# Performance work log

Measured on AMD Instinct MI355X. Metric: run time of the kernel, lower is better.

Reference implementation:

```python
import jax, jax.numpy as jnp
import numpy as np

NUM_HEADS = 16

def setup_inputs() -> dict:
    key = jax.random.key(0)
    kq, kk, kv = jax.random.split(key, 3)
    B, S, D = 4, 2048, 1024
    return {
        "queries": jax.random.normal(kq, (B, S, D), dtype=jnp.float32),
        "keys": jax.random.normal(kk, (B, S, D), dtype=jnp.float32),
        "values": jax.random.normal(kv, (B, S, D), dtype=jnp.float32),
    }

def _split_heads(x):
    # [B, S, D] -> [B, H, S, Dh]
    B, S, D = x.shape
    return x.reshape(B, S, NUM_HEADS, D // NUM_HEADS).transpose(0, 2, 1, 3)

def reference(queries, keys, values):
    q = _split_heads(queries)   # [B, H, S, Dh]
    k = _split_heads(keys)
    v = _split_heads(values)
    d_k = k.shape[-1]
    scale = 1.0 / jnp.sqrt(jnp.asarray(d_k, dtype=q.dtype))
    # [B, H, S, S] score matrix (materialized, as in the original bmm path)
    scores = jnp.einsum('bhqd,bhkd->bhqk', q, k) * scale
    weights = jax.nn.softmax(scores, axis=-1)
    out = jnp.einsum('bhqk,bhkd->bhqd', weights, v)  # [B, H, S, Dh]
    B, H, S, Dh = out.shape
    return out.transpose(0, 2, 1, 3).reshape(B, S, H * Dh)
```

## Files before the change

kernel.cpp:

```cpp
#include <hip/hip_runtime.h>
#include <hip/hip_bf16.h>
#include <math.h>

#define SEQ    2048
#define NH     16
#define DH     64
#define DMODEL 1024
#define KT     64
#define NT     (SEQ/KT)
#define KH_BYTES (4 * NH * SEQ * DH * 2)

typedef __bf16 bf16x8 __attribute__((ext_vector_type(8)));
typedef float  f32x4  __attribute__((ext_vector_type(4)));
typedef float  f32x16 __attribute__((ext_vector_type(16)));
typedef unsigned u32x2 __attribute__((ext_vector_type(2)));
typedef unsigned short u16x8 __attribute__((ext_vector_type(8)));
typedef __attribute__((address_space(3))) unsigned int        lds_u32_t;
typedef __attribute__((address_space(1))) const unsigned int  g_u32_t;

__device__ __forceinline__ ushort f2bf(float f) {
    union { __hip_bfloat16 h; ushort u; } z;
    z.h = __float2bfloat16(f);
    return z.u;
}

__device__ __forceinline__ unsigned pk2(float lo, float hi) {
    unsigned r;
    asm("v_cvt_pk_bf16_f32 %0, %1, %2" : "=v"(r) : "v"(lo), "v"(hi));
    return r;
}

__device__ __forceinline__ float fexp2(float x) {
#if __has_builtin(__builtin_amdgcn_exp2f)
    return __builtin_amdgcn_exp2f(x);
#else
    float r; asm("v_exp_f32 %0, %1\n\ts_nop 0" : "=v"(r) : "v"(x)); return r;
#endif
}

__device__ __forceinline__ void load16(const char* g, char* l) {
    __builtin_amdgcn_global_load_lds((g_u32_t*)g, (lds_u32_t*)l, 16, 0, 0);
}

__global__ __launch_bounds__(256)
void prep_kv(const float* __restrict__ K, const float* __restrict__ V,
             ushort* __restrict__ Kh, ushort* __restrict__ Vt) {
    __shared__ __attribute__((aligned(16))) ushort T[64 * 64];
    int blk = blockIdx.x;
    int tid = threadIdx.x;
    if (blk < 2048) {
        int i = tid >> 6;
        int c = tid & 63;
        int g = blk * 4 + i;
        int b = g >> 11, s = g & 2047;
        int h = c >> 2, d0 = (c & 3) * 16;
        const float* kp = K + (size_t)g * DMODEL + c * 16;
        float4 f0 = ((const float4*)kp)[0];
        float4 f1 = ((const float4*)kp)[1];
        float4 f2 = ((const float4*)kp)[2];
        float4 f3 = ((const float4*)kp)[3];
        u16x8 a, bq;
        a[0]=f2bf(f0.x); a[1]=f2bf(f0.y); a[2]=f2bf(f0.z); a[3]=f2bf(f0.w);
        a[4]=f2bf(f1.x); a[5]=f2bf(f1.y); a[6]=f2bf(f1.z); a[7]=f2bf(f1.w);
        bq[0]=f2bf(f2.x); bq[1]=f2bf(f2.y); bq[2]=f2bf(f2.z); bq[3]=f2bf(f2.w);
        bq[4]=f2bf(f3.x); bq[5]=f2bf(f3.y); bq[6]=f2bf(f3.z); bq[7]=f2bf(f3.w);
        ushort* op = Kh + ((size_t)(b * NH + h) * SEQ + s) * DH + d0;
        *(u16x8*)op = a;
        *(u16x8*)(op + 8) = bq;
    } else {
        int vb = blk - 2048;
        int st = vb & 31, bh = vb >> 5;
        int b = bh >> 4, h = bh & 15;
        int s0 = st * 64;
        char* TB = (char*)T;
        {
            int sr = tid >> 2, seg = tid & 3;
            const float* vp = V + ((size_t)(b * SEQ + s0 + sr)) * DMODEL + h * DH + seg * 16;
            float4 f0 = ((const float4*)vp)[0];
            float4 f1 = ((const float4*)vp)[1];
            float4 f2 = ((const float4*)vp)[2];
            float4 f3 = ((const float4*)vp)[3];
            union { unsigned u[4]; u16x8 v; } za, zb;
            za.u[0] = pk2(f0.x, f0.y); za.u[1] = pk2(f0.z, f0.w);
            za.u[2] = pk2(f1.x, f1.y); za.u[3] = pk2(f1.z, f1.w);
            zb.u[0] = pk2(f2.x, f2.y); zb.u[1] = pk2(f2.z, f2.w);
            zb.u[2] = pk2(f3.x, f3.y); zb.u[3] = pk2(f3.z, f3.w);
            int base = sr * 128 + seg * 32;
            int sw = (sr & 7) << 4;
            *(u16x8*)(TB + ((base) ^ sw))      = za.v;
            *(u16x8*)(TB + ((base + 16) ^ sw)) = zb.v;
        }
        __syncthreads();
        {
            int dr = tid >> 2, sseg = tid & 3;
            u16x8 o0, o1;
            #pragma unroll
            for (int i = 0; i < 8; ++i) {
                int s = sseg * 16 + i;
                o0[i] = *(const ushort*)(TB + ((s * 128 + dr * 2) ^ ((s & 7) << 4)));
            }
            #pragma unroll
            for (int i = 0; i < 8; ++i) {
                int s = sseg * 16 + 8 + i;
                o1[i] = *(const ushort*)(TB + ((s * 128 + dr * 2) ^ ((s & 7) << 4)));
            }
            ushort* op = Vt + ((size_t)(bh * DH + dr)) * SEQ + s0 + sseg * 16;
            *(u16x8*)op = o0;
            *(u16x8*)(op + 8) = o1;
        }
    }
}

__global__ __launch_bounds__(256, 2)
void mha_fwd32(const float* __restrict__ Q, const ushort* __restrict__ Kh,
               const ushort* __restrict__ Vt, float* __restrict__ Out) {
    int raw = blockIdx.x;
    int bid = (raw & 7) * 64 + (raw >> 3);
    int qt = bid & 7;
    int bh = bid >> 3;
    int b = bh >> 4, h = bh & 15;

    const int tid  = threadIdx.x;
    const int lane = tid & 63;
    const int w    = tid >> 6;
    const int l31  = lane & 31;
    const int lh   = lane >> 5;

    __shared__ __attribute__((aligned(16))) ushort Ks[2][KT * DH];
    __shared__ __attribute__((aligned(16))) ushort Vs[2][KT * DH];

    int o0  = tid * 16;
    int o1  = o0 + 4096;
    int so0 = o0 ^ (((o0 >> 7) & 7) << 4);
    int so1 = o1 ^ (((o1 >> 7) & 7) << 4);
    const char* khead = (const char*)Kh + (size_t)bh * (SEQ * DH * 2);
    const char* vhead = (const char*)Vt + (size_t)bh * (SEQ * DH * 2);
    const char* kg0 = khead + so0;
    const char* kg1 = khead + so1;
    const char* vg0 = vhead + (size_t)(o0 >> 7) * (SEQ * 2) + (so0 & 127);
    const char* vg1 = vhead + (size_t)(o1 >> 7) * (SEQ * 2) + (so1 & 127);

    const float QSCALE = 0.125f * 1.4426950408889634f;
    bf16x8 qf[2][4];
    #pragma unroll
    for (int q2 = 0; q2 < 2; ++q2) {
        int qrow = qt * 256 + w * 64 + q2 * 32 + l31;
        const float* qp = Q + ((size_t)b * SEQ + qrow) * DMODEL + h * DH + lh * 8;
        #pragma unroll
        for (int ks = 0; ks < 4; ++ks) {
            float4 fa = *(const float4*)(qp + ks * 16);
            float4 fb = *(const float4*)(qp + ks * 16 + 4);
            union { unsigned u[4]; bf16x8 v; } z;
            z.u[0] = pk2(fa.x * QSCALE, fa.y * QSCALE);
            z.u[1] = pk2(fa.z * QSCALE, fa.w * QSCALE);
            z.u[2] = pk2(fb.x * QSCALE, fb.y * QSCALE);
            z.u[3] = pk2(fb.z * QSCALE, fb.w * QSCALE);
            qf[q2][ks] = z.v;
        }
    }

    f32x16 zro;
    #pragma unroll
    for (int i = 0; i < 16; ++i) zro[i] = 0.f;
    bf16x8 onesf;
    {
        union { unsigned u[4]; bf16x8 v; } z;
        z.u[0] = 0x3F803F80u; z.u[1] = 0x3F803F80u;
        z.u[2] = 0x3F803F80u; z.u[3] = 0x3F803F80u;
        onesf = z.v;
    }

    f32x16 oacc[2][2];
    #pragma unroll
    for (int a = 0; a < 2; ++a)
        #pragma unroll
        for (int d = 0; d < 2; ++d)
            #pragma unroll
            for (int i = 0; i < 16; ++i) oacc[a][d][i] = 0.f;
    f32x16 lacc[2];
    #pragma unroll
    for (int a = 0; a < 2; ++a)
        #pragma unroll
        for (int i = 0; i < 16; ++i) lacc[a][i] = 0.f;

    int swz = (l31 & 7) << 4;
    int offRd[2][4];
    #pragma unroll
    for (int x = 0; x < 2; ++x)
        #pragma unroll
        for (int ks = 0; ks < 4; ++ks)
            offRd[x][ks] = (x * 32 + l31) * 128 + ((ks * 32 + lh * 16) ^ swz);

    {
        char* kb = (char*)&Ks[0][0] + w * 1024;
        char* vb = (char*)&Vs[0][0] + w * 1024;
        load16(kg0, kb); load16(kg1, kb + 4096);
        load16(vg0, vb); load16(vg1, vb + 4096);
        kg0 += KT * DH * 2; kg1 += KT * DH * 2; vg0 += KT * 2; vg1 += KT * 2;
    }
    __syncthreads();

    int buf = 0;
    for (int kt = 0; kt < NT; ++kt) {
        if (kt + 1 < NT) {
            char* kb = (char*)&Ks[buf ^ 1][0] + w * 1024;
            char* vb = (char*)&Vs[buf ^ 1][0] + w * 1024;
            load16(kg0, kb); load16(kg1, kb + 4096);
            load16(vg0, vb); load16(vg1, vb + 4096);
            kg0 += KT * DH * 2; kg1 += KT * DH * 2; vg0 += KT * 2; vg1 += KT * 2;
        }
        const char* kbb = (const char*)&Ks[buf][0];
        const char* vbb = (const char*)&Vs[buf][0];

        f32x16 sc[2][2];
        __builtin_amdgcn_s_setprio(1);
        #pragma unroll
        for (int t = 0; t < 2; ++t) {
            #pragma unroll
            for (int ks = 0; ks < 4; ++ks) {
                bf16x8 kf = *(const bf16x8*)(kbb + offRd[t][ks]);
                if (ks == 0) {
                    sc[0][t] = __builtin_amdgcn_mfma_f32_32x32x16_bf16(kf, qf[0][0], zro, 0, 0, 0);
                    sc[1][t] = __builtin_amdgcn_mfma_f32_32x32x16_bf16(kf, qf[1][0], zro, 0, 0, 0);
                } else {
                    sc[0][t] = __builtin_amdgcn_mfma_f32_32x32x16_bf16(kf, qf[0][ks], sc[0][t], 0, 0, 0);
                    sc[1][t] = __builtin_amdgcn_mfma_f32_32x32x16_bf16(kf, qf[1][ks], sc[1][t], 0, 0, 0);
                }
            }
        }
        __builtin_amdgcn_s_setprio(0);

        bf16x8 pa[2][4];
        #pragma unroll
        for (int q2 = 0; q2 < 2; ++q2) {
            float e[2][16];
            #pragma unroll
            for (int t = 0; t < 2; ++t)
                #pragma unroll
                for (int r = 0; r < 16; ++r)
                    e[t][r] = fexp2(sc[q2][t][r]);
            #pragma unroll
            for (int t = 0; t < 2; ++t) {
                #pragma unroll
                for (int s = 0; s < 2; ++s) {
                    unsigned X  = pk2(e[t][8 * s + 0], e[t][8 * s + 1]);
                    unsigned Bw = pk2(e[t][8 * s + 2], e[t][8 * s + 3]);
                    unsigned Y  = pk2(e[t][8 * s + 4], e[t][8 * s + 5]);
                    unsigned Dw = pk2(e[t][8 * s + 6], e[t][8 * s + 7]);
                    u32x2 pq = __builtin_amdgcn_permlane32_swap(X, Y, false, false);
                    u32x2 rs = __builtin_amdgcn_permlane32_swap(Bw, Dw, false, false);
                    union { unsigned u[4]; bf16x8 v; } z;
                    z.u[0] = pq.x; z.u[1] = rs.x; z.u[2] = pq.y; z.u[3] = rs.y;
                    pa[q2][2 * t + s] = z.v;
                }
            }
        }

        __builtin_amdgcn_s_setprio(1);
        #pragma unroll
        for (int dt = 0; dt < 2; ++dt) {
            #pragma unroll
            for (int ks = 0; ks < 4; ++ks) {
                bf16x8 vf = *(const bf16x8*)(vbb + offRd[dt][ks]);
                oacc[0][dt] = __builtin_amdgcn_mfma_f32_32x32x16_bf16(pa[0][ks], vf, oacc[0][dt], 0, 0, 0);
                oacc[1][dt] = __builtin_amdgcn_mfma_f32_32x32x16_bf16(pa[1][ks], vf, oacc[1][dt], 0, 0, 0);
            }
        }
        #pragma unroll
        for (int ks = 0; ks < 4; ++ks) {
            lacc[0] = __builtin_amdgcn_mfma_f32_32x32x16_bf16(pa[0][ks], onesf, lacc[0], 0, 0, 0);
            lacc[1] = __builtin_amdgcn_mfma_f32_32x32x16_bf16(pa[1][ks], onesf, lacc[1], 0, 0, 0);
        }
        __builtin_amdgcn_s_setprio(0);

        __syncthreads();
        buf ^= 1;
    }

    #pragma unroll
    for (int q2 = 0; q2 < 2; ++q2) {
        #pragma unroll
        for (int r = 0; r < 16; ++r) {
            float rl = __builtin_amdgcn_rcpf(lacc[q2][r]);
            int qp_ = (r & 3) + 8 * (r >> 2) + 4 * lh;
            int qrow = qt * 256 + w * 64 + q2 * 32 + qp_;
            float* op = Out + ((size_t)b * SEQ + qrow) * DMODEL + h * DH + l31;
            op[0]  = oacc[q2][0][r] * rl;
            op[32] = oacc[q2][1][r] * rl;
        }
    }
}

__global__ __launch_bounds__(256)
void mha_fwd_fallback(const float* __restrict__ Q, const float* __restrict__ K,
                      const float* __restrict__ V, float* __restrict__ Out) {
    int raw = blockIdx.x;
    int bid = (raw & 7) * 256 + (raw >> 3);
    int qt = bid & 31;
    int bh = bid >> 5;
    int b  = bh >> 4;
    int h  = bh & 15;
    const int tid  = threadIdx.x;
    const int lane = tid & 63;
    const int w    = tid >> 6;
    const int l15  = lane & 15;
    const int g    = lane >> 4;
    __shared__ ushort KsS[KT * DH];
    __shared__ ushort VTS[KT * DH];
    __shared__ ushort PlS[4][16 * KT];
    char* KsB = (char*)KsS;
    char* VTB = (char*)VTS;
    char* PlB = (char*)&PlS[w][0];
    const size_t base = ((size_t)b * SEQ) * DMODEL + (size_t)h * DH;
    const float QSCALE = 0.125f * 1.4426950408889634f;
    bf16x8 qa[2];
    {
        int qrow = qt * 64 + w * 16 + l15;
        const float* qp = Q + base + (size_t)qrow * DMODEL;
        for (int ds = 0; ds < 2; ++ds) {
            float4 f0 = *(const float4*)(qp + ds * 32 + g * 8);
            float4 f1 = *(const float4*)(qp + ds * 32 + g * 8 + 4);
            union { ushort u[8]; bf16x8 v; } pk;
            pk.u[0] = f2bf(f0.x * QSCALE); pk.u[1] = f2bf(f0.y * QSCALE);
            pk.u[2] = f2bf(f0.z * QSCALE); pk.u[3] = f2bf(f0.w * QSCALE);
            pk.u[4] = f2bf(f1.x * QSCALE); pk.u[5] = f2bf(f1.y * QSCALE);
            pk.u[6] = f2bf(f1.z * QSCALE); pk.u[7] = f2bf(f1.w * QSCALE);
            qa[ds] = pk.v;
        }
    }
    f32x4 oacc[4];
    for (int i = 0; i < 4; ++i) { oacc[i][0]=0.f; oacc[i][1]=0.f; oacc[i][2]=0.f; oacc[i][3]=0.f; }
    float m_r[4], l_r[4];
    for (int r = 0; r < 4; ++r) { m_r[r] = -3.0e38f; l_r[r] = 0.f; }
    for (int kt = 0; kt < SEQ / KT; ++kt) {
        const int kbase = kt * KT;
        for (int i = 0; i < 4; ++i) {
            int pos  = i * 256 + tid;
            int krow = pos >> 4;
            int d4   = (pos & 15) * 4;
            const float* kp = K + base + (size_t)(kbase + krow) * DMODEL + d4;
            float4 f = *(const float4*)kp;
            ushort4 u = make_ushort4(f2bf(f.x), f2bf(f.y), f2bf(f.z), f2bf(f.w));
            int off = (krow * 128 + d4 * 2) ^ ((krow & 7) << 4);
            *(ushort4*)(KsB + off) = u;
        }
        {
            int kg = tid >> 4;
            int d4 = (tid & 15) * 4;
            const float* vp = V + base + (size_t)(kbase + kg * 4) * DMODEL + d4;
            float4 r0 = *(const float4*)(vp);
            float4 r1 = *(const float4*)(vp + DMODEL);
            float4 r2 = *(const float4*)(vp + 2 * DMODEL);
            float4 r3 = *(const float4*)(vp + 3 * DMODEL);
            ushort4 c0 = make_ushort4(f2bf(r0.x), f2bf(r1.x), f2bf(r2.x), f2bf(r3.x));
            ushort4 c1 = make_ushort4(f2bf(r0.y), f2bf(r1.y), f2bf(r2.y), f2bf(r3.y));
            ushort4 c2 = make_ushort4(f2bf(r0.z), f2bf(r1.z), f2bf(r2.z), f2bf(r3.z));
            ushort4 c3 = make_ushort4(f2bf(r0.w), f2bf(r1.w), f2bf(r2.w), f2bf(r3.w));
            int row, off;
            row = d4 + 0; off = (row * 128 + kg * 8) ^ ((row & 7) << 4); *(ushort4*)(VTB + off) = c0;
            row = d4 + 1; off = (row * 128 + kg * 8) ^ ((row & 7) << 4); *(ushort4*)(VTB + off) = c1;
            row = d4 + 2; off = (row * 128 + kg * 8) ^ ((row & 7) << 4); *(ushort4*)(VTB + off) = c2;
            row = d4 + 3; off = (row * 128 + kg * 8) ^ ((row & 7) << 4); *(ushort4*)(VTB + off) = c3;
        }
        __syncthreads();
        f32x4 sc[4];
        for (int sub = 0; sub < 4; ++sub) {
            f32x4 a; a[0]=0.f; a[1]=0.f; a[2]=0.f; a[3]=0.f;
            for (int ds = 0; ds < 2; ++ds) {
                int krow = sub * 16 + l15;
                int off = (krow * 128 + ds * 64 + g * 16) ^ ((krow & 7) << 4);
                bf16x8 kb = *(const bf16x8*)(KsB + off);
                a = __builtin_amdgcn_mfma_f32_16x16x32_bf16(qa[ds], kb, a, 0, 0, 0);
            }
            sc[sub] = a;
        }
        float corr[4];
        float p[4][4];
        for (int r = 0; r < 4; ++r) {
            float t = fmaxf(fmaxf(sc[0][r], sc[1][r]), fmaxf(sc[2][r], sc[3][r]));
            t = fmaxf(t, __shfl_xor(t, 1));
            t = fmaxf(t, __shfl_xor(t, 2));
            t = fmaxf(t, __shfl_xor(t, 4));
            t = fmaxf(t, __shfl_xor(t, 8));
            float mn = fmaxf(m_r[r], t);
            corr[r] = exp2f(m_r[r] - mn);
            m_r[r] = mn;
            float s = 0.f;
            for (int sub = 0; sub < 4; ++sub) {
                float e = exp2f(sc[sub][r] - mn);
                p[sub][r] = e;
                s += e;
            }
            s += __shfl_xor(s, 1);
            s += __shfl_xor(s, 2);
            s += __shfl_xor(s, 4);
            s += __shfl_xor(s, 8);
            l_r[r] = l_r[r] * corr[r] + s;
        }
        for (int dsub = 0; dsub < 4; ++dsub)
            for (int r = 0; r < 4; ++r)
                oacc[dsub][r] *= corr[r];
        for (int r = 0; r < 4; ++r) {
            int row = g * 4 + r;
            for (int sub = 0; sub < 4; ++sub) {
                int off = (row * 128 + (sub * 16 + l15) * 2) ^ ((row & 7) << 4);
                *(ushort*)(PlB + off) = f2bf(p[sub][r]);
            }
        }
        bf16x8 pa[2];
        for (int ks = 0; ks < 2; ++ks) {
            int off = (l15 * 128 + ks * 64 + g * 16) ^ ((l15 & 7) << 4);
            pa[ks] = *(const bf16x8*)(PlB + off);
        }
        for (int dsub = 0; dsub < 4; ++dsub) {
            f32x4 a = oacc[dsub];
            for (int ks = 0; ks < 2; ++ks) {
                int row = dsub * 16 + l15;
                int off = (row * 128 + ks * 64 + g * 16) ^ ((row & 7) << 4);
                bf16x8 vb = *(const bf16x8*)(VTB + off);
                a = __builtin_amdgcn_mfma_f32_16x16x32_bf16(pa[ks], vb, a, 0, 0, 0);
            }
            oacc[dsub] = a;
        }
        __syncthreads();
    }
    for (int r = 0; r < 4; ++r) {
        float rl = 1.0f / l_r[r];
        int qrow = qt * 64 + w * 16 + g * 4 + r;
        float* op = Out + ((size_t)b * SEQ + qrow) * DMODEL + (size_t)h * DH;
        for (int dsub = 0; dsub < 4; ++dsub)
            op[dsub * 16 + l15] = oacc[dsub][r] * rl;
    }
}

extern "C" void kernel_launch(void* const* d_in, const int* in_sizes, int n_in,
                              void* d_out, int out_size, void* d_ws, size_t ws_size,
                              hipStream_t stream) {
    const float* Q = (const float*)d_in[0];
    const float* K = (const float*)d_in[1];
    const float* V = (const float*)d_in[2];
    float* Out = (float*)d_out;

    if (ws_size >= (size_t)2 * KH_BYTES) {
        ushort* Kh = (ushort*)d_ws;
        ushort* Vt = (ushort*)((char*)d_ws + KH_BYTES);
        prep_kv<<<dim3(4096), dim3(256), 0, stream>>>(K, V, Kh, Vt);
        mha_fwd32<<<dim3(512), dim3(256), 0, stream>>>(Q, Kh, Vt, Out);
    } else {
        mha_fwd_fallback<<<dim3(2048), dim3(256), 0, stream>>>(Q, K, V, Out);
    }
}
```

Before: 200.8 us.

## Store V transposed in contiguous per-tile blocks and unify K/V prep blocks

```diff
diff --git a/kernel.cpp b/kernel.cpp
--- a/kernel.cpp
+++ b/kernel.cpp
@@ -45,69 +45,62 @@
 __global__ __launch_bounds__(256)
 void prep_kv(const float* __restrict__ K, const float* __restrict__ V,
              ushort* __restrict__ Kh, ushort* __restrict__ Vt) {
-    __shared__ __attribute__((aligned(16))) ushort T[64 * 64];
+    __shared__ __attribute__((aligned(16))) unsigned T[64 * 32];
     int blk = blockIdx.x;
     int tid = threadIdx.x;
-    if (blk < 2048) {
-        int i = tid >> 6;
-        int c = tid & 63;
-        int g = blk * 4 + i;
-        int b = g >> 11, s = g & 2047;
-        int h = c >> 2, d0 = (c & 3) * 16;
-        const float* kp = K + (size_t)g * DMODEL + c * 16;
-        float4 f0 = ((const float4*)kp)[0];
-        float4 f1 = ((const float4*)kp)[1];
-        float4 f2 = ((const float4*)kp)[2];
-        float4 f3 = ((const float4*)kp)[3];
-        u16x8 a, bq;
-        a[0]=f2bf(f0.x); a[1]=f2bf(f0.y); a[2]=f2bf(f0.z); a[3]=f2bf(f0.w);
-        a[4]=f2bf(f1.x); a[5]=f2bf(f1.y); a[6]=f2bf(f1.z); a[7]=f2bf(f1.w);
-        bq[0]=f2bf(f2.x); bq[1]=f2bf(f2.y); bq[2]=f2bf(f2.z); bq[3]=f2bf(f2.w);
-        bq[4]=f2bf(f3.x); bq[5]=f2bf(f3.y); bq[6]=f2bf(f3.z); bq[7]=f2bf(f3.w);
-        ushort* op = Kh + ((size_t)(b * NH + h) * SEQ + s) * DH + d0;
-        *(u16x8*)op = a;
-        *(u16x8*)(op + 8) = bq;
+    int isV = blk >> 11;
+    int tix = blk & 2047;
+    int st = tix & 31, bh = tix >> 5;
+    int b = bh >> 4, h = bh & 15;
+    int s0 = st * 64;
+    int sr  = tid >> 2;
+    int seg = tid & 3;
+
+    const float* ip = (isV ? V : K) + ((size_t)(b * SEQ + s0 + sr)) * DMODEL + h * DH + seg * 16;
+    float4 f0 = ((const float4*)ip)[0];
+    float4 f1 = ((const float4*)ip)[1];
+    float4 f2 = ((const float4*)ip)[2];
+    float4 f3 = ((const float4*)ip)[3];
+    unsigned wv[8];
+    wv[0] = pk2(f0.x, f0.y); wv[1] = pk2(f0.z, f0.w);
+    wv[2] = pk2(f1.x, f1.y); wv[3] = pk2(f1.z, f1.w);
+    wv[4] = pk2(f2.x, f2.y); wv[5] = pk2(f2.z, f2.w);
+    wv[6] = pk2(f3.x, f3.y); wv[7] = pk2(f3.z, f3.w);
+
+    if (!isV) {
+        union { unsigned u[4]; u16x8 v; } a, c;
+        a.u[0]=wv[0]; a.u[1]=wv[1]; a.u[2]=wv[2]; a.u[3]=wv[3];
+        c.u[0]=wv[4]; c.u[1]=wv[5]; c.u[2]=wv[6]; c.u[3]=wv[7];
+        ushort* op = Kh + ((size_t)bh * SEQ + s0 + sr) * DH + seg * 16;
+        *(u16x8*)op = a.v;
+        *(u16x8*)(op + 8) = c.v;
     } else {
-        int vb = blk - 2048;
-        int st = vb & 31, bh = vb >> 5;
-        int b = bh >> 4, h = bh & 15;
-        int s0 = st * 64;
-        char* TB = (char*)T;
-        {
-            int sr = tid >> 2, seg = tid & 3;
-            const float* vp = V + ((size_t)(b * SEQ + s0 + sr)) * DMODEL + h * DH + seg * 16;
-            float4 f0 = ((const float4*)vp)[0];
-            float4 f1 = ((const float4*)vp)[1];
-            float4 f2 = ((const float4*)vp)[2];
-            float4 f3 = ((const float4*)vp)[3];
-            union { unsigned u[4]; u16x8 v; } za, zb;
-            za.u[0] = pk2(f0.x, f0.y); za.u[1] = pk2(f0.z, f0.w);
-            za.u[2] = pk2(f1.x, f1.y); za.u[3] = pk2(f1.z, f1.w);
-            zb.u[0] = pk2(f2.x, f2.y); zb.u[1] = pk2(f2.z, f2.w);
-            zb.u[2] = pk2(f3.x, f3.y); zb.u[3] = pk2(f3.z, f3.w);
-            int base = sr * 128 + seg * 32;
-            int sw = (sr & 7) << 4;
-            *(u16x8*)(TB + ((base) ^ sw))      = za.v;
-            *(u16x8*)(TB + ((base + 16) ^ sw)) = zb.v;
+        int key = sr & 31;
+        #pragma unroll
+        for (int j = 0; j < 8; ++j) {
+            int pos = (seg * 8 + j) ^ key;
+            T[sr * 32 + pos] = wv[j];
         }
         __syncthreads();
-        {
-            int dr = tid >> 2, sseg = tid & 3;
-            u16x8 o0, o1;
-            #pragma unroll
-            for (int i = 0; i < 8; ++i) {
-                int s = sseg * 16 + i;
-                o0[i] = *(const ushort*)(TB + ((s * 128 + dr * 2) ^ ((s & 7) << 4)));
-            }
-            #pragma unroll
-            for (int i = 0; i < 8; ++i) {
-                int s = sseg * 16 + 8 + i;
-                o1[i] = *(const ushort*)(TB + ((s * 128 + dr * 2) ^ ((s & 7) << 4)));
-            }
-            ushort* op = Vt + ((size_t)(bh * DH + dr)) * SEQ + s0 + sseg * 16;
-            *(u16x8*)op = o0;
-            *(u16x8*)(op + 8) = o1;
-        }
+        int dr = sr;
+        int sseg = seg;
+        const char* TB = (const char*)T;
+        u16x8 o0, o1;
+        #pragma unroll
+        for (int i = 0; i < 8; ++i) {
+            int s = sseg * 16 + i;
+            int off = s * 128 + ((((dr >> 1) ^ (s & 31)) << 2) | ((dr & 1) << 1));
+            o0[i] = *(const ushort*)(TB + off);
+        }
+        #pragma unroll
+        for (int i = 0; i < 8; ++i) {
+            int s = sseg * 16 + 8 + i;
+            int off = s * 128 + ((((dr >> 1) ^ (s & 31)) << 2) | ((dr & 1) << 1));
+            o1[i] = *(const ushort*)(TB + off);
+        }
+        ushort* op = Vt + (size_t)bh * (SEQ * DH) + st * (64 * 64) + dr * 64 + sseg * 16;
+        *(u16x8*)op = o0;
+        *(u16x8*)(op + 8) = o1;
     }
 }
 
@@ -137,8 +130,8 @@
     const char* vhead = (const char*)Vt + (size_t)bh * (SEQ * DH * 2);
     const char* kg0 = khead + so0;
     const char* kg1 = khead + so1;
-    const char* vg0 = vhead + (size_t)(o0 >> 7) * (SEQ * 2) + (so0 & 127);
-    const char* vg1 = vhead + (size_t)(o1 >> 7) * (SEQ * 2) + (so1 & 127);
+    const char* vg0 = vhead + so0;
+    const char* vg1 = vhead + so1;
 
     const float QSCALE = 0.125f * 1.4426950408889634f;
     bf16x8 qf[2][4];
@@ -196,7 +189,7 @@
         char* vb = (char*)&Vs[0][0] + w * 1024;
         load16(kg0, kb); load16(kg1, kb + 4096);
         load16(vg0, vb); load16(vg1, vb + 4096);
-        kg0 += KT * DH * 2; kg1 += KT * DH * 2; vg0 += KT * 2; vg1 += KT * 2;
+        kg0 += KT * DH * 2; kg1 += KT * DH * 2; vg0 += KT * DH * 2; vg1 += KT * DH * 2;
     }
     __syncthreads();
 
@@ -207,7 +200,7 @@
             char* vb = (char*)&Vs[buf ^ 1][0] + w * 1024;
             load16(kg0, kb); load16(kg1, kb + 4096);
             load16(vg0, vb); load16(vg1, vb + 4096);
-            kg0 += KT * DH * 2; kg1 += KT * DH * 2; vg0 += KT * 2; vg1 += KT * 2;
+            kg0 += KT * DH * 2; kg1 += KT * DH * 2; vg0 += KT * DH * 2; vg1 += KT * DH * 2;
         }
         const char* kbb = (const char*)&Ks[buf][0];
         const char* vbb = (const char*)&Vs[buf][0];
```

After: 200.1 us. Within noise of the previous version (-0.4%).
